# Performance work log

Measured on AMD Instinct MI355X. Metric: run time of the kernel, lower is better.

Reference implementation:

```python
import jax, jax.numpy as jnp
import numpy as np
import math

HIDDEN, HEADS, D_K = 768, 12, 64
BS, SEQ = 4, 2048


def setup_inputs() -> dict:
    key = jax.random.key(0)
    ks = jax.random.split(key, 5)
    s = 1.0 / math.sqrt(HIDDEN)
    return {
        "x": jax.random.normal(ks[0], (BS, SEQ, HIDDEN), dtype=jnp.float32),
        "Wq": jax.random.normal(ks[1], (HIDDEN, HIDDEN), dtype=jnp.float32) * s,
        "bq": jnp.zeros((HIDDEN,), jnp.float32),
        "Wk": jax.random.normal(ks[2], (HIDDEN, HIDDEN), dtype=jnp.float32) * s,
        "bk": jnp.zeros((HIDDEN,), jnp.float32),
        "Wv": jax.random.normal(ks[3], (HIDDEN, HIDDEN), dtype=jnp.float32) * s,
        "bv": jnp.zeros((HIDDEN,), jnp.float32),
        "Wo": jax.random.normal(ks[4], (HIDDEN, HIDDEN), dtype=jnp.float32) * s,
        "bo": jnp.zeros((HIDDEN,), jnp.float32),
    }


def reference(x, Wq, bq, Wk, bk, Wv, bv, Wo, bo):
    bs, seq, _ = x.shape
    # projections; nn.Linear computes x @ W.T + b
    def proj(W, b):
        y = jnp.einsum("bsd,ed->bse", x, W) + b
        return y.reshape(bs, seq, HEADS, D_K).transpose(0, 2, 1, 3)  # [b,h,s,d]
    q, k, v = proj(Wq, bq), proj(Wk, bk), proj(Wv, bv)
    scores = jnp.einsum("bhqd,bhkd->bhqk", q, k) / jnp.sqrt(jnp.float32(D_K))
    attn = jax.nn.softmax(scores, axis=-1)  # dropout = 0 (eval)
    ctx = jnp.einsum("bhqk,bhkd->bhqd", attn, v)
    ctx = ctx.transpose(0, 2, 1, 3).reshape(bs, seq, HIDDEN)
    return jnp.einsum("bsd,ed->bse", ctx, Wo) + bo
```

## Files before the change

### kernel.cpp

```cpp
#include <hip/hip_runtime.h>
#include <hip/hip_bf16.h>

#define HID 768
#define NHEAD 12
#define DKH 64
#define BSZ 4
#define SEQ 2048
#define MTOT (BSZ*SEQ)
#define NBH (BSZ*NHEAD)

typedef __attribute__((ext_vector_type(8))) short   s16x8;
typedef __attribute__((ext_vector_type(8))) __bf16  bf16x8;
typedef __attribute__((ext_vector_type(4))) __bf16  bf16x4;
typedef __attribute__((ext_vector_type(4))) float   f32x4;

#define MFMA16x32(A,B,C) __builtin_amdgcn_mfma_f32_16x16x32_bf16((A),(B),(C),0,0,0)

__device__ __forceinline__ unsigned short f2bf(float f) {
  union { float f; unsigned int u; } a; a.f = f;
  return (unsigned short)((a.u + 0x7FFFu + ((a.u >> 16) & 1u)) >> 16);
}

__device__ __forceinline__ void gload_lds16(const unsigned short* g, unsigned short* l) {
  __builtin_amdgcn_global_load_lds((const __attribute__((address_space(1))) void*)g,
                                   (__attribute__((address_space(3))) void*)l, 16, 0, 0);
}

__global__ __launch_bounds__(256) void cvt_kernel(const float* __restrict__ src,
                                                  unsigned short* __restrict__ dst, int n) {
  int i = (blockIdx.x * 256 + threadIdx.x) * 4;
  if (i >= n) return;
  float4 v = *(const float4*)(src + i);
  ushort4 o;
  o.x = f2bf(v.x); o.y = f2bf(v.y); o.z = f2bf(v.z); o.w = f2bf(v.w);
  *(ushort4*)(dst + i) = o;
}

__global__ __launch_bounds__(256) void cvtw_kernel(const float* __restrict__ s0,
                                                   const float* __restrict__ s1,
                                                   const float* __restrict__ s2,
                                                   const float* __restrict__ s3,
                                                   unsigned short* __restrict__ dst) {
  const float* s = (blockIdx.y == 0) ? s0 : (blockIdx.y == 1) ? s1 : (blockIdx.y == 2) ? s2 : s3;
  int i = (blockIdx.x * 256 + threadIdx.x) * 4;
  float4 v = *(const float4*)(s + i);
  ushort4 o;
  o.x = f2bf(v.x); o.y = f2bf(v.y); o.z = f2bf(v.z); o.w = f2bf(v.w);
  *(ushort4*)(dst + (size_t)blockIdx.y * HID * HID + i) = o;
}

#define GEMM_STEP(CUR, KTN, DOPREF)                                         \
  {                                                                         \
    if (DOPREF) {                                                           \
      _Pragma("unroll")                                                     \
      for (int i = 0; i < 4; ++i) {                                         \
        const int c = wave * 4 + i;                                         \
        gload_lds16(Aptr + (size_t)(c*8 + sr) * HID + (KTN) + sc8,          \
                    As[(CUR)^1] + c*512);                                   \
        gload_lds16(Wptr + (size_t)(c*8 + sr) * HID + (KTN) + sc8,          \
                    Bs[(CUR)^1] + c*512);                                   \
      }                                                                     \
    }                                                                       \
    const char* ab = (const char*)As[CUR];                                  \
    const char* bb = (const char*)Bs[CUR];                                  \
    _Pragma("unroll")                                                       \
    for (int kk = 0; kk < 2; ++kk) {                                        \
      bf16x8 af[4], bfr[4];                                                 \
      _Pragma("unroll")                                                     \
      for (int mb = 0; mb < 4; ++mb) {                                      \
        const int r = wm + mb*16 + l16;                                     \
        af[mb] = *(const bf16x8*)(ab + r*128 + (((kk*4 + lg) ^ (l16 & 7)) << 4)); \
      }                                                                     \
      _Pragma("unroll")                                                     \
      for (int nb = 0; nb < 4; ++nb) {                                      \
        const int r = wn + nb*16 + l16;                                     \
        bfr[nb] = *(const bf16x8*)(bb + r*128 + (((kk*4 + lg) ^ (l16 & 7)) << 4)); \
      }                                                                     \
      _Pragma("unroll")                                                     \
      for (int mb = 0; mb < 4; ++mb)                                        \
        _Pragma("unroll")                                                   \
        for (int nb = 0; nb < 4; ++nb)                                      \
          acc[mb][nb] = MFMA16x32(af[mb], bfr[nb], acc[mb][nb]);            \
    }                                                                       \
    __syncthreads();                                                        \
  }

template<int MODE>
__global__ __launch_bounds__(256) void gemm_kernel(
    const unsigned short* __restrict__ A,
    const unsigned short* __restrict__ W,
    const float* __restrict__ bias0,
    const float* __restrict__ bias1,
    const float* __restrict__ bias2,
    void* __restrict__ out_raw,
    unsigned short* __restrict__ vtimg)
{
  __shared__ unsigned short As[2][128*64];
  __shared__ unsigned short Bs[2][128*64];
  const int tid  = threadIdx.x;
  const int wave = tid >> 6, lane = tid & 63;
  const int l16  = lane & 15, lg = lane >> 4;
  const int f    = blockIdx.x;
  const int xcd  = f & 7, rr = f >> 3;
  const int bx   = xcd*8 + (rr & 7), by = rr >> 3;
  const int m0   = bx * 128, n0 = by * 128;
  const int wm   = (wave & 1) * 64,  wn = (wave >> 1) * 64;

  const f32x4 z4 = {0.f, 0.f, 0.f, 0.f};
  f32x4 acc[4][4];
#pragma unroll
  for (int i = 0; i < 4; ++i)
#pragma unroll
    for (int j = 0; j < 4; ++j) acc[i][j] = z4;

  const int sr  = lane >> 3;
  const int sc8 = ((lane & 7) ^ sr) << 3;
  const unsigned short* Aptr = A + (size_t)m0 * HID;
  const unsigned short* Wptr = W + (size_t)n0 * HID;

#pragma unroll
  for (int i = 0; i < 4; ++i) {
    const int c = wave * 4 + i;
    gload_lds16(Aptr + (size_t)(c*8 + sr) * HID + sc8, As[0] + c*512);
    gload_lds16(Wptr + (size_t)(c*8 + sr) * HID + sc8, Bs[0] + c*512);
  }
  __syncthreads();

#pragma unroll 1
  for (int tt = 0; tt < 6; ++tt) {
    GEMM_STEP(0, (2*tt+1)*64, true)
    GEMM_STEP(1, (2*tt+2)*64, (tt < 5))
  }

  if (MODE == 0) {
    unsigned short* out = (unsigned short*)out_raw;
    const float QSCALE = 0.18033688011112042f;
    const int which = (n0 + wn) / HID;
    if (which == 2) {
      const int h = (n0 + wn - 2*HID) >> 6;
#pragma unroll
      for (int nb = 0; nb < 4; ++nb) {
        const int d = nb*16 + l16;
        const float bias = bias2[h*64 + d];
#pragma unroll
        for (int mb = 0; mb < 4; ++mb) {
          const int m    = m0 + wm + mb*16 + lg*4;
          const int b    = m >> 11, s = m & (SEQ - 1);
          const int tile = s >> 6;
          const int slot = ((s & 63) >> 2) ^ l16;
          ushort4 w;
          w.x = f2bf(acc[mb][nb][0] + bias);
          w.y = f2bf(acc[mb][nb][1] + bias);
          w.z = f2bf(acc[mb][nb][2] + bias);
          w.w = f2bf(acc[mb][nb][3] + bias);
          *(ushort4*)(vtimg + ((((size_t)(b*NHEAD + h)*32 + tile)*64 + d)*64 + slot*4)) = w;
        }
      }
    } else {
      const float* bp  = (which == 0) ? bias0 : bias1;
      const float scl  = (which == 0) ? QSCALE : 1.0f;
      const int e_base = n0 + wn - which*HID;
#pragma unroll
      for (int nb = 0; nb < 4; ++nb) {
        const int e = e_base + nb*16 + l16;
        const float bias = bp[e];
        const int h = e >> 6, d = e & 63;
#pragma unroll
        for (int mb = 0; mb < 4; ++mb)
#pragma unroll
          for (int j = 0; j < 4; ++j) {
            const int m = m0 + wm + mb*16 + lg*4 + j;
            const int b = m >> 11, s = m & (SEQ - 1);
            const float v = (acc[mb][nb][j] + bias) * scl;
            out[((((size_t)which*BSZ + b)*NHEAD + h)*SEQ + s)*DKH + d] = f2bf(v);
          }
      }
    }
  } else {
    float* out = (float*)out_raw;
#pragma unroll
    for (int nb = 0; nb < 4; ++nb) {
      const int n = n0 + wn + nb*16 + l16;
      const float bias = bias0[n];
#pragma unroll
      for (int mb = 0; mb < 4; ++mb)
#pragma unroll
        for (int j = 0; j < 4; ++j) {
          const int m = m0 + wm + mb*16 + lg*4 + j;
          out[(size_t)m*HID + n] = acc[mb][nb][j] + bias;
        }
    }
  }
}

#define ATTN_STEP(CUR, DOPREF)                                              \
  {                                                                         \
    if (DOPREF) {                                                           \
      gload_lds16(kSrc0, Ks[(CUR)^1] + wave*1024);                          \
      gload_lds16(kSrc1, Ks[(CUR)^1] + wave*1024 + 512);                    \
      gload_lds16(vSrc0, Vs[(CUR)^1] + wave*1024);                          \
      gload_lds16(vSrc1, Vs[(CUR)^1] + wave*1024 + 512);                    \
      kSrc0 += 64*DKH; kSrc1 += 64*DKH; vSrc0 += 4096; vSrc1 += 4096;       \
    }                                                                       \
    const char* kb = (const char*)Ks[CUR];                                  \
    const char* vb = (const char*)Vs[CUR];                                  \
    f32x4 sc[2][4];                                                         \
    __builtin_amdgcn_s_setprio(1);                                          \
    _Pragma("unroll")                                                       \
    for (int nb = 0; nb < 4; ++nb) {                                        \
      bf16x8 kf0 = *(const bf16x8*)(kb + kbase0 + nb*2048);                 \
      bf16x8 kf1 = *(const bf16x8*)(kb + kbase1 + nb*2048);                 \
      f32x4 z0 = z4, z1 = z4;                                               \
      z0 = MFMA16x32(kf0, qf[0][0], z0);                                    \
      z0 = MFMA16x32(kf1, qf[0][1], z0);                                    \
      z1 = MFMA16x32(kf0, qf[1][0], z1);                                    \
      z1 = MFMA16x32(kf1, qf[1][1], z1);                                    \
      sc[0][nb] = z0; sc[1][nb] = z1;                                       \
    }                                                                       \
    __builtin_amdgcn_s_setprio(0);                                          \
    bf16x8 pa[2][2];                                                        \
    _Pragma("unroll")                                                       \
    for (int qa = 0; qa < 2; ++qa)                                          \
      _Pragma("unroll")                                                     \
      for (int nb = 0; nb < 4; ++nb)                                        \
        _Pragma("unroll")                                                   \
        for (int j = 0; j < 4; ++j)                                         \
          pa[qa][nb>>1][(nb&1)*4 + j] =                                     \
            (__bf16)__builtin_amdgcn_exp2f(sc[qa][nb][j]);                  \
    __builtin_amdgcn_s_setprio(1);                                          \
    csum[0] = MFMA16x32(pa[0][0], ones, csum[0]);                           \
    csum[0] = MFMA16x32(pa[0][1], ones, csum[0]);                           \
    csum[1] = MFMA16x32(pa[1][0], ones, csum[1]);                           \
    csum[1] = MFMA16x32(pa[1][1], ones, csum[1]);                           \
    _Pragma("unroll")                                                       \
    for (int db = 0; db < 4; ++db) {                                        \
      bf16x4 v00 = *(const bf16x4*)(vb + vbase0 + db*2048);                 \
      bf16x4 v01 = *(const bf16x4*)(vb + vbase1 + db*2048);                 \
      bf16x4 v10 = *(const bf16x4*)(vb + vbase2 + db*2048);                 \
      bf16x4 v11 = *(const bf16x4*)(vb + vbase3 + db*2048);                 \
      bf16x8 vf0 = __builtin_shufflevector(v00, v01, 0,1,2,3,4,5,6,7);      \
      bf16x8 vf1 = __builtin_shufflevector(v10, v11, 0,1,2,3,4,5,6,7);      \
      cacc[0][db] = MFMA16x32(pa[0][0], vf0, cacc[0][db]);                  \
      cacc[0][db] = MFMA16x32(pa[0][1], vf1, cacc[0][db]);                  \
      cacc[1][db] = MFMA16x32(pa[1][0], vf0, cacc[1][db]);                  \
      cacc[1][db] = MFMA16x32(pa[1][1], vf1, cacc[1][db]);                  \
    }                                                                       \
    __builtin_amdgcn_s_setprio(0);                                          \
    __syncthreads();                                                        \
  }

__global__ __launch_bounds__(256, 3) void attn_kernel(const unsigned short* __restrict__ qkv,
                                                      const unsigned short* __restrict__ vtimg,
                                                      unsigned short* __restrict__ ctx)
{
  __shared__ unsigned short Ks[2][64*64];
  __shared__ unsigned short Vs[2][64*64];
  const int tid  = threadIdx.x;
  const int wave = tid >> 6, lane = tid & 63;
  const int l16  = lane & 15, lg = lane >> 4;
  const int f   = blockIdx.x;
  const int xcd = f & 7, idx = f >> 3;
  const int bh  = xcd * 6 + (idx >> 4);
  const int qt  = idx & 15;
  const int b   = bh / NHEAD, h = bh - b * NHEAD;
  const int q0  = qt * 128 + wave * 32;

  const unsigned short* Qg = qkv + (size_t)bh * (SEQ*DKH);
  const unsigned short* Kg = qkv + (size_t)(NBH + bh) * (SEQ*DKH);

  const int srow  = lane >> 3;
  const int scolK = ((lane & 7) ^ srow) << 3;
  const unsigned short* kSrc0 = Kg + (size_t)(wave*16 + srow) * DKH + scolK;
  const unsigned short* kSrc1 = Kg + (size_t)(wave*16 + 8 + srow) * DKH + scolK;
  const unsigned short* vSrc0 = vtimg + ((size_t)bh*32*64 + wave*16 + srow) * 64 + (lane & 7) * 8;
  const unsigned short* vSrc1 = vSrc0 + 8*64;

  const int kbase0 = l16*128 + ((lg ^ (l16 & 7)) << 4);
  const int kbase1 = l16*128 + (((lg + 4) ^ (l16 & 7)) << 4);
  const int vbase0 = l16*128 + (((lg     ) ^ l16) << 3);
  const int vbase1 = l16*128 + (((lg +  4) ^ l16) << 3);
  const int vbase2 = l16*128 + (((lg +  8) ^ l16) << 3);
  const int vbase3 = l16*128 + (((lg + 12) ^ l16) << 3);

  bf16x8 qf[2][2];
#pragma unroll
  for (int qa = 0; qa < 2; ++qa) {
    qf[qa][0] = *(const bf16x8*)(Qg + (size_t)(q0 + qa*16 + l16)*DKH + lg*8);
    qf[qa][1] = *(const bf16x8*)(Qg + (size_t)(q0 + qa*16 + l16)*DKH + 32 + lg*8);
  }

  bf16x8 ones;
#pragma unroll
  for (int e = 0; e < 8; ++e) ones[e] = (__bf16)1.0f;

  const f32x4 z4 = {0.f,0.f,0.f,0.f};
  f32x4 cacc[2][4];
  f32x4 csum[2] = {z4, z4};
#pragma unroll
  for (int qa = 0; qa < 2; ++qa)
#pragma unroll
    for (int db = 0; db < 4; ++db) cacc[qa][db] = z4;

  gload_lds16(kSrc0, Ks[0] + wave*1024);
  gload_lds16(kSrc1, Ks[0] + wave*1024 + 512);
  gload_lds16(vSrc0, Vs[0] + wave*1024);
  gload_lds16(vSrc1, Vs[0] + wave*1024 + 512);
  kSrc0 += 64*DKH; kSrc1 += 64*DKH; vSrc0 += 4096; vSrc1 += 4096;
  __syncthreads();

#pragma unroll 1
  for (int tt = 0; tt < 16; ++tt) {
    ATTN_STEP(0, true)
    ATTN_STEP(1, (tt < 15))
  }

#pragma unroll
  for (int qa = 0; qa < 2; ++qa) {
    f32x4 inv;
#pragma unroll
    for (int j = 0; j < 4; ++j) inv[j] = 1.0f / csum[qa][j];
#pragma unroll
    for (int db = 0; db < 4; ++db)
#pragma unroll
      for (int j = 0; j < 4; ++j) {
        const int srow2 = q0 + qa*16 + lg*4 + j;
        ctx[((size_t)(b*SEQ + srow2))*HID + h*DKH + db*16 + l16] = f2bf(cacc[qa][db][j] * inv[j]);
      }
  }
}

extern "C" void kernel_launch(void* const* d_in, const int* in_sizes, int n_in,
                              void* d_out, int out_size, void* d_ws, size_t ws_size,
                              hipStream_t stream) {
  (void)in_sizes; (void)n_in; (void)out_size; (void)ws_size;
  const float* x  = (const float*)d_in[0];
  const float* Wq = (const float*)d_in[1];
  const float* bq = (const float*)d_in[2];
  const float* Wk = (const float*)d_in[3];
  const float* bk = (const float*)d_in[4];
  const float* Wv = (const float*)d_in[5];
  const float* bv = (const float*)d_in[6];
  const float* Wo = (const float*)d_in[7];
  const float* bo = (const float*)d_in[8];

  unsigned short* ws   = (unsigned short*)d_ws;
  unsigned short* Xb   = ws;
  unsigned short* Wqkv = Xb + (size_t)MTOT * HID;
  unsigned short* Wob  = Wqkv + (size_t)3 * HID * HID;
  unsigned short* qkvb = Wob + (size_t)HID * HID;
  unsigned short* vtb  = qkvb + (size_t)2 * NBH * SEQ * DKH;
  unsigned short* ctxb = Xb;

  cvt_kernel<<<(MTOT*HID)/1024, 256, 0, stream>>>(x, Xb, MTOT*HID);
  cvtw_kernel<<<dim3((HID*HID)/1024, 4), 256, 0, stream>>>(Wq, Wk, Wv, Wo, Wqkv);

  gemm_kernel<0><<<1152, 256, 0, stream>>>(Xb, Wqkv, bq, bk, bv, qkvb, vtb);
  attn_kernel<<<768, 256, 0, stream>>>(qkvb, vtb, ctxb);
  gemm_kernel<1><<<384, 256, 0, stream>>>(ctxb, Wob, bo, nullptr, nullptr, d_out, nullptr);
}
```

Before: 130.8 us.

## Merge conversion kernels and parametrize GEMM N-tile width per launch

Combines the activation and weight fp32-to-bf16 conversions into one launch, removing a kernel launch and its tail. Templates the GEMM on the N-tile width: the QKV projection now uses 128x192 tiles over 768 blocks and the output projection uses 128x96 tiles over 512 blocks. The aim is better wave quantization across the CUs and more reuse of the A tile in the QKV GEMM, at the cost of more accumulator registers and a larger LDS footprint for NB=6, which may lower occupancy. The V-transpose epilogue now derives the head per column to handle tiles that span heads.

```diff
diff --git a/kernel.cpp b/kernel.cpp
--- a/kernel.cpp
+++ b/kernel.cpp
@@ -26,29 +26,32 @@
                                    (__attribute__((address_space(3))) void*)l, 16, 0, 0);
 }
 
-__global__ __launch_bounds__(256) void cvt_kernel(const float* __restrict__ src,
-                                                  unsigned short* __restrict__ dst, int n) {
-  int i = (blockIdx.x * 256 + threadIdx.x) * 4;
-  if (i >= n) return;
+__global__ __launch_bounds__(256) void cvtall_kernel(const float* __restrict__ x,
+                                                     const float* __restrict__ w0,
+                                                     const float* __restrict__ w1,
+                                                     const float* __restrict__ w2,
+                                                     const float* __restrict__ w3,
+                                                     unsigned short* __restrict__ xb,
+                                                     unsigned short* __restrict__ wb) {
+  const int bid = blockIdx.x;
+  const float* src; unsigned short* dst; int off;
+  if (bid < 6144) {
+    src = x; dst = xb; off = bid * 1024;
+  } else {
+    const int t = bid - 6144;
+    const int wi = t / 576;
+    const int ro = t - wi * 576;
+    src = (wi == 0) ? w0 : (wi == 1) ? w1 : (wi == 2) ? w2 : w3;
+    dst = wb + (size_t)wi * HID * HID;
+    off = ro * 1024;
+  }
+  const int i = off + threadIdx.x * 4;
   float4 v = *(const float4*)(src + i);
   ushort4 o;
   o.x = f2bf(v.x); o.y = f2bf(v.y); o.z = f2bf(v.z); o.w = f2bf(v.w);
   *(ushort4*)(dst + i) = o;
 }
 
-__global__ __launch_bounds__(256) void cvtw_kernel(const float* __restrict__ s0,
-                                                   const float* __restrict__ s1,
-                                                   const float* __restrict__ s2,
-                                                   const float* __restrict__ s3,
-                                                   unsigned short* __restrict__ dst) {
-  const float* s = (blockIdx.y == 0) ? s0 : (blockIdx.y == 1) ? s1 : (blockIdx.y == 2) ? s2 : s3;
-  int i = (blockIdx.x * 256 + threadIdx.x) * 4;
-  float4 v = *(const float4*)(s + i);
-  ushort4 o;
-  o.x = f2bf(v.x); o.y = f2bf(v.y); o.z = f2bf(v.z); o.w = f2bf(v.w);
-  *(ushort4*)(dst + (size_t)blockIdx.y * HID * HID + i) = o;
-}
-
 #define GEMM_STEP(CUR, KTN, DOPREF)                                         \
   {                                                                         \
     if (DOPREF) {                                                           \
@@ -57,6 +60,10 @@
         const int c = wave * 4 + i;                                         \
         gload_lds16(Aptr + (size_t)(c*8 + sr) * HID + (KTN) + sc8,          \
                     As[(CUR)^1] + c*512);                                   \
+      }                                                                     \
+      _Pragma("unroll")                                                     \
+      for (int i = 0; i < NB; ++i) {                                        \
+        const int c = wave * NB + i;                                        \
         gload_lds16(Wptr + (size_t)(c*8 + sr) * HID + (KTN) + sc8,          \
                     Bs[(CUR)^1] + c*512);                                   \
       }                                                                     \
@@ -65,27 +72,27 @@
     const char* bb = (const char*)Bs[CUR];                                  \
     _Pragma("unroll")                                                       \
     for (int kk = 0; kk < 2; ++kk) {                                        \
-      bf16x8 af[4], bfr[4];                                                 \
+      bf16x8 af[4], bfr[NB];                                                \
       _Pragma("unroll")                                                     \
       for (int mb = 0; mb < 4; ++mb) {                                      \
         const int r = wm + mb*16 + l16;                                     \
         af[mb] = *(const bf16x8*)(ab + r*128 + (((kk*4 + lg) ^ (l16 & 7)) << 4)); \
       }                                                                     \
       _Pragma("unroll")                                                     \
-      for (int nb = 0; nb < 4; ++nb) {                                      \
+      for (int nb = 0; nb < NB; ++nb) {                                     \
         const int r = wn + nb*16 + l16;                                     \
         bfr[nb] = *(const bf16x8*)(bb + r*128 + (((kk*4 + lg) ^ (l16 & 7)) << 4)); \
       }                                                                     \
       _Pragma("unroll")                                                     \
       for (int mb = 0; mb < 4; ++mb)                                        \
         _Pragma("unroll")                                                   \
-        for (int nb = 0; nb < 4; ++nb)                                      \
+        for (int nb = 0; nb < NB; ++nb)                                     \
           acc[mb][nb] = MFMA16x32(af[mb], bfr[nb], acc[mb][nb]);            \
     }                                                                       \
     __syncthreads();                                                        \
   }
 
-template<int MODE>
+template<int MODE, int NB>
 __global__ __launch_bounds__(256) void gemm_kernel(
     const unsigned short* __restrict__ A,
     const unsigned short* __restrict__ W,
@@ -96,22 +103,22 @@
     unsigned short* __restrict__ vtimg)
 {
   __shared__ unsigned short As[2][128*64];
-  __shared__ unsigned short Bs[2][128*64];
+  __shared__ unsigned short Bs[2][NB*32*64];
   const int tid  = threadIdx.x;
   const int wave = tid >> 6, lane = tid & 63;
   const int l16  = lane & 15, lg = lane >> 4;
   const int f    = blockIdx.x;
   const int xcd  = f & 7, rr = f >> 3;
   const int bx   = xcd*8 + (rr & 7), by = rr >> 3;
-  const int m0   = bx * 128, n0 = by * 128;
-  const int wm   = (wave & 1) * 64,  wn = (wave >> 1) * 64;
+  const int m0   = bx * 128, n0 = by * (NB*32);
+  const int wm   = (wave & 1) * 64,  wn = (wave >> 1) * (NB*16);
 
   const f32x4 z4 = {0.f, 0.f, 0.f, 0.f};
-  f32x4 acc[4][4];
+  f32x4 acc[4][NB];
 #pragma unroll
   for (int i = 0; i < 4; ++i)
 #pragma unroll
-    for (int j = 0; j < 4; ++j) acc[i][j] = z4;
+    for (int j = 0; j < NB; ++j) acc[i][j] = z4;
 
   const int sr  = lane >> 3;
   const int sc8 = ((lane & 7) ^ sr) << 3;
@@ -122,6 +129,10 @@
   for (int i = 0; i < 4; ++i) {
     const int c = wave * 4 + i;
     gload_lds16(Aptr + (size_t)(c*8 + sr) * HID + sc8, As[0] + c*512);
+  }
+#pragma unroll
+  for (int i = 0; i < NB; ++i) {
+    const int c = wave * NB + i;
     gload_lds16(Wptr + (size_t)(c*8 + sr) * HID + sc8, Bs[0] + c*512);
   }
   __syncthreads();
@@ -137,11 +148,12 @@
     const float QSCALE = 0.18033688011112042f;
     const int which = (n0 + wn) / HID;
     if (which == 2) {
-      const int h = (n0 + wn - 2*HID) >> 6;
-#pragma unroll
-      for (int nb = 0; nb < 4; ++nb) {
-        const int d = nb*16 + l16;
-        const float bias = bias2[h*64 + d];
+      const int e_base = n0 + wn - 2*HID;
+#pragma unroll
+      for (int nb = 0; nb < NB; ++nb) {
+        const int e = e_base + nb*16 + l16;
+        const int h = e >> 6, d = e & 63;
+        const float bias = bias2[e];
 #pragma unroll
         for (int mb = 0; mb < 4; ++mb) {
           const int m    = m0 + wm + mb*16 + lg*4;
@@ -161,7 +173,7 @@
       const float scl  = (which == 0) ? QSCALE : 1.0f;
       const int e_base = n0 + wn - which*HID;
 #pragma unroll
-      for (int nb = 0; nb < 4; ++nb) {
+      for (int nb = 0; nb < NB; ++nb) {
         const int e = e_base + nb*16 + l16;
         const float bias = bp[e];
         const int h = e >> 6, d = e & 63;
@@ -179,7 +191,7 @@
   } else {
     float* out = (float*)out_raw;
 #pragma unroll
-    for (int nb = 0; nb < 4; ++nb) {
+    for (int nb = 0; nb < NB; ++nb) {
       const int n = n0 + wn + nb*16 + l16;
       const float bias = bias0[n];
 #pragma unroll
@@ -351,10 +363,9 @@
   unsigned short* vtb  = qkvb + (size_t)2 * NBH * SEQ * DKH;
   unsigned short* ctxb = Xb;
 
-  cvt_kernel<<<(MTOT*HID)/1024, 256, 0, stream>>>(x, Xb, MTOT*HID);
-  cvtw_kernel<<<dim3((HID*HID)/1024, 4), 256, 0, stream>>>(Wq, Wk, Wv, Wo, Wqkv);
-
-  gemm_kernel<0><<<1152, 256, 0, stream>>>(Xb, Wqkv, bq, bk, bv, qkvb, vtb);
+  cvtall_kernel<<<6144 + 4*576, 256, 0, stream>>>(x, Wq, Wk, Wv, Wo, Xb, Wqkv);
+
+  gemm_kernel<0,6><<<768, 256, 0, stream>>>(Xb, Wqkv, bq, bk, bv, qkvb, vtb);
   attn_kernel<<<768, 256, 0, stream>>>(qkvb, vtb, ctxb);
-  gemm_kernel<1><<<384, 256, 0, stream>>>(ctxb, Wob, bo, nullptr, nullptr, d_out, nullptr);
-}
+  gemm_kernel<1,3><<<512, 256, 0, stream>>>(ctxb, Wob, bo, nullptr, nullptr, d_out, nullptr);
+}
```

Result: slower. 136.7 us (+4.6%).
